# Optimization experiments

Hardware: AMD Instinct MI355X
Metric: run time of the kernel (lower is better)

Reference implementation:

```python
import jax, jax.numpy as jnp
import numpy as np
from jax import lax

BITWIDTH = 7
EPS = 1e-5


def ti_quant(x):
    """TiFloatToInt8: per-tensor int8 quantization with power-of-2 scale."""
    rng = jnp.max(jnp.abs(x))
    bw = jnp.ceil(jnp.log2(rng))
    exp = bw - BITWIDTH
    q = jnp.clip(jnp.round(x * 2.0 ** (BITWIDTH - bw)), -128.0, 127.0)
    return q, exp


def ti_conv(xv, xe, wv, we, pad):
    """TiConv2d: integer conv (simulated in f32, all values int-valued),
    int32 accumulate, then shift back to 8 bits; exponents add."""
    acc = lax.conv_general_dilated(
        xv, wv, window_strides=(1, 1), padding=[(pad, pad), (pad, pad)],
        dimension_numbers=("NCHW", "OIHW", "NCHW"))
    rng = jnp.max(jnp.abs(acc))
    bw = jnp.ceil(jnp.log2(rng))
    shift = jnp.maximum(bw - BITWIDTH, 0.0)
    q = jnp.clip(jnp.round(acc * 2.0 ** (-shift)), -128.0, 127.0)
    return q, xe + we + shift


def batchnorm(x, gamma, beta):
    # training-mode BN: batch statistics over (N, H, W)
    mean = jnp.mean(x, axis=(0, 2, 3), keepdims=True)
    var = jnp.var(x, axis=(0, 2, 3), keepdims=True)
    g = gamma[None, :, None, None]
    b = beta[None, :, None, None]
    return g * (x - mean) * lax.rsqrt(var + EPS) + b


def setup_inputs() -> dict:
    key = jax.random.key(0)
    k0, k1, k2, k3, k4 = jax.random.split(key, 5)
    B, Cin, Cout, H, W = 32, 128, 256, 56, 56
    x_val = jax.random.randint(k0, (B, Cin, H, W), -128, 128, dtype=jnp.int32)
    x_exp = jnp.zeros((), jnp.float32) - 7.0
    wDW = jnp.round(jnp.clip(jax.random.normal(k1, (Cin, Cin, 3, 3), jnp.float32) * 32.0, -128.0, 127.0))
    wDW_exp = jnp.zeros((), jnp.float32) - 9.0
    wPW = jnp.round(jnp.clip(jax.random.normal(k2, (Cout, Cin, 1, 1), jnp.float32) * 32.0, -128.0, 127.0))
    wPW_exp = jnp.zeros((), jnp.float32) - 9.0
    gamma1 = jnp.ones((Cin,), jnp.float32) + 0.1 * jax.random.normal(k3, (Cin,), jnp.float32)
    beta1 = jnp.zeros((Cin,), jnp.float32)
    gamma2 = jnp.ones((Cout,), jnp.float32) + 0.1 * jax.random.normal(k4, (Cout,), jnp.float32)
    beta2 = jnp.zeros((Cout,), jnp.float32)
    return {"x_val": x_val, "x_exp": x_exp, "wDW": wDW, "wDW_exp": wDW_exp,
            "wPW": wPW, "wPW_exp": wPW_exp, "gamma1": gamma1, "beta1": beta1,
            "gamma2": gamma2, "beta2": beta2}


def reference(x_val, x_exp, wDW, wDW_exp, wPW, wPW_exp, gamma1, beta1, gamma2, beta2):
    xv = x_val.astype(jnp.float32)
    # convDW (3x3, in->in, pad=1)
    q, e = ti_conv(xv, x_exp, wDW, wDW_exp, 1)
    # dequant -> bn1 -> quant
    f = batchnorm(q * 2.0 ** e, gamma1, beta1)
    q, e = ti_quant(f)
    # TiReLU on int values
    q = jnp.maximum(q, 0.0)
    # convPW (1x1, in->out)
    q, e = ti_conv(q, e, wPW, wPW_exp, 0)
    # dequant -> bn2 -> quant -> relu
    f = batchnorm(q * 2.0 ** e, gamma2, beta2)
    q, e = ti_quant(f)
    q = jnp.maximum(q, 0.0)
    return q.astype(jnp.int8), e
```

## Files before the change

### kernel.cpp

```cpp
#include <hip/hip_runtime.h>
#include <cstdint>
#include <cstddef>

#define C1 128
#define C2 256
#define Hh 56
#define Wd 56
#define HW 3136
#define NHW 100352
#define N1 ((size_t)12845056)
#define N2 ((size_t)25690112)
#define XPSZ ((size_t)13778944)
#define NREP 8
#define NB1 392

typedef int v4i __attribute__((ext_vector_type(4)));
typedef int v16i __attribute__((ext_vector_type(16)));

static constexpr size_t OFF_XP = 0;
static constexpr size_t OFF_Q1 = XPSZ;
static constexpr size_t OFF_Q3 = OFF_Q1 + N1;
static constexpr size_t OFF_WQ1 = OFF_Q3 + N2;
static constexpr size_t OFF_WQ2 = OFF_WQ1 + 147456;
static constexpr size_t OFF_STATS = OFF_WQ2 + 32768;

struct Stats {
  int absmax1, absmax2, pad0, pad1;
  float scale1, e1, s2, e2;
  float scaleq2, e3, sf, ef;
  int padA[20];
  int tick1, padB[31];
  int tick2, padC[31];
  int tick3, padD[31];
  int sum1[NREP][C1]; unsigned sumsq1[NREP][C1];
  int min1[NREP][C1], max1[NREP][C1];
  float A1[C1], B1c[C1];
  int sum2[NREP][C2]; unsigned sumsq2[NREP][C2];
  int min2[NREP][C2], max2[NREP][C2];
  float A2[C2], B2c[C2];
};

__global__ __launch_bounds__(256) void k_pre(
    const int* __restrict__ x, signed char* __restrict__ xp,
    const float* __restrict__ wDW, signed char* __restrict__ wq1t,
    const float* __restrict__ wPW, signed char* __restrict__ wq2t,
    Stats* st) {
  __shared__ signed char lds[56 * 132];
  int t = threadIdx.x, bid = blockIdx.x;
  if (bid < 1856) {
    int hh = bid % 58, n = bid / 58;
    int* xpw = (int*)(xp + ((size_t)n * 58 + hh) * 7424);
    if (hh == 0 || hh == 57) {
      for (int o = t; o < 1856; o += 256) xpw[o] = 0;
      return;
    }
    int h = hh - 1;
    const int* xb = x + (size_t)n * C1 * HW + h * 56;
    for (int idx = t; idx < 7168; idx += 256) {
      int c = idx / 56, w = idx - c * 56;
      lds[w * 132 + c] = (signed char)xb[(size_t)c * HW + w];
    }
    __syncthreads();
    for (int o = t; o < 1856; o += 256) {
      int kb = o / 232, r = o - kb * 232, ww = r >> 2, cw = r & 3;
      int val = (ww == 0 || ww == 57) ? 0
                : *(const int*)&lds[(ww - 1) * 132 + kb * 16 + cw * 4];
      xpw[o] = val;
    }
    return;
  }
  if (bid < 2432) {
    int idx = (bid - 1856) * 256 + t;
    int co = idx / 1152, r = idx - co * 1152;
    int ci = r / 9, pos = r - ci * 9;
    int k = pos * 128 + ci;
    wq1t[(size_t)(k >> 4) * 2048 + co * 16 + (k & 15)] = (signed char)(int)wDW[idx];
    return;
  }
  if (bid < 2560) {
    int i = (bid - 2432) * 256 + t;
    int co = i >> 7, ci = i & 127;
    wq2t[(size_t)(ci >> 4) * 4096 + co * 16 + (ci & 15)] = (signed char)(int)wPW[i];
    return;
  }
  if (t == 0) {
    st->absmax1 = 0; st->absmax2 = 0;
    st->tick1 = 0; st->tick2 = 0; st->tick3 = 0;
  }
  for (int c = t; c < NREP * C1; c += 256) {
    ((int*)st->sum1)[c] = 0; ((unsigned*)st->sumsq1)[c] = 0u;
    ((int*)st->min1)[c] = 127; ((int*)st->max1)[c] = -128;
  }
  for (int c = t; c < NREP * C2; c += 256) {
    ((int*)st->sum2)[c] = 0; ((unsigned*)st->sumsq2)[c] = 0u;
    ((int*)st->min2)[c] = 127; ((int*)st->max2)[c] = -128;
  }
}

__device__ inline v4i ld16_lds(const signed char* p) {
  const int2* q = (const int2*)p;
  int2 lo = q[0], hi = q[1];
  v4i r; r[0] = lo.x; r[1] = lo.y; r[2] = hi.x; r[3] = hi.y;
  return r;
}

__device__ inline float bn_affine_v(int sum, unsigned sumsq, int mn, int mx,
                                    float g, float b, float e_in,
                                    float* Aout, float* Bout) {
  double meanq = (double)sum / (double)NHW;
  double varq = (double)sumsq / (double)NHW - meanq * meanq;
  float se = exp2f(e_in);
  float mean = (float)meanq * se;
  float var = (float)varq * se * se;
  float rsq = 1.0f / sqrtf(var + 1e-5f);
  float Avv = g * se * rsq;
  float Bvv = b - g * mean * rsq;
  *Aout = Avv; *Bout = Bvv;
  return fmaxf(fabsf(Avv * (float)mn + Bvv), fabsf(Avv * (float)mx + Bvv));
}

__device__ inline void conv1_mfma(const signed char* __restrict__ xp,
                                  const signed char* __restrict__ wq1t,
                                  int bx, int t, v16i a1[2][4]) {
  int lane = t & 63, wave = t >> 6;
  int half = lane >> 5, l31 = lane & 31;
  size_t g0 = (size_t)bx * 256;

  const signed char* ab[2];
#pragma unroll
  for (int i = 0; i < 2; ++i) {
    size_t gm = g0 + wave * 64 + i * 32 + l31;
    int n = (int)(gm / HW);
    int p = (int)(gm - (size_t)n * HW);
    int h = p / 56, w = p - h * 56;
    ab[i] = xp + ((size_t)n * 58 + h) * 7424 + w * 16 + half * 928;
  }
  const signed char* bb[4];
#pragma unroll
  for (int j = 0; j < 4; ++j)
    bb[j] = wq1t + (size_t)(j * 32 + l31) * 16 + half * 2048;

#pragma unroll
  for (int i = 0; i < 2; ++i)
#pragma unroll
    for (int j = 0; j < 4; ++j)
#pragma unroll
      for (int r = 0; r < 16; ++r) a1[i][j][r] = 0;

#pragma unroll
  for (int pos = 0; pos < 9; ++pos) {
    int kh = pos / 3, kw = pos - kh * 3;
    const signed char* a0p = ab[0] + kh * 7424 + kw * 16;
    const signed char* a1p = ab[1] + kh * 7424 + kw * 16;
#pragma unroll
    for (int kb = 0; kb < 8; kb += 2) {
      v4i af0 = *(const v4i*)(a0p + kb * 928);
      v4i af1 = *(const v4i*)(a1p + kb * 928);
      v4i bf[4];
#pragma unroll
      for (int j = 0; j < 4; ++j)
        bf[j] = *(const v4i*)(bb[j] + pos * 16384 + kb * 2048);
#pragma unroll
      for (int j = 0; j < 4; ++j) {
        a1[0][j] = __builtin_amdgcn_mfma_i32_32x32x32_i8(af0, bf[j], a1[0][j], 0, 0, 0);
        a1[1][j] = __builtin_amdgcn_mfma_i32_32x32x32_i8(af1, bf[j], a1[1][j], 0, 0, 0);
      }
    }
  }
}

__global__ __launch_bounds__(256, 2) void k_conv1f(
    const signed char* __restrict__ xp, const signed char* __restrict__ wq1t,
    signed char* __restrict__ q1, Stats* st,
    const float* __restrict__ x_exp, const float* __restrict__ wDW_exp,
    const float* __restrict__ gamma1, const float* __restrict__ beta1) {
  __shared__ int reda[4];
  __shared__ int vbro;
  __shared__ int qti[256 * 34];
  __shared__ int psum[C1], psq[C1], pmn[C1], pmx[C1];
  __shared__ float redc[2];
  __shared__ int lastf;
  signed char* qt = (signed char*)qti;
  int t = threadIdx.x, lane = t & 63, wave = t >> 6;
  int half = lane >> 5, l31 = lane & 31;
  int rep = blockIdx.x & (NREP - 1);

  v16i a1[2][4];
  conv1_mfma(xp, wq1t, blockIdx.x, t, a1);

  int am = 0;
#pragma unroll
  for (int i = 0; i < 2; ++i)
#pragma unroll
    for (int j = 0; j < 4; ++j)
#pragma unroll
      for (int r = 0; r < 16; ++r) am = max(am, abs(a1[i][j][r]));
  for (int off = 32; off; off >>= 1) am = max(am, __shfl_down(am, off, 64));
  if (lane == 0) reda[wave] = am;
  if (t < C1) { psum[t] = 0; psq[t] = 0; pmn[t] = 127; pmx[t] = -128; }
  __syncthreads();
  if (t == 0)
    atomicMax(&st->absmax1, max(max(reda[0], reda[1]), max(reda[2], reda[3])));
  __syncthreads();

  if (t == 0) {
    atomicAdd(&st->tick1, 1);
    while (atomicAdd(&st->tick1, 0) < NB1)
      __builtin_amdgcn_s_sleep(8);
    vbro = atomicAdd(&st->absmax1, 0);
  }
  __syncthreads();

  int v1 = vbro;
  int pw = 31 - __clz(v1 | 1);
  int bw = ((v1 & (v1 - 1)) == 0) ? pw : pw + 1;
  int sh = max(bw - 7, 0);
  float scale1 = exp2f((float)(-sh));
  float e1 = x_exp[0] + wDW_exp[0] + (float)sh;
  if (blockIdx.x == 0 && t == 0) st->e1 = e1;

#pragma unroll
  for (int j = 0; j < 4; ++j) {
    int sj = 0, sqj = 0, mnj = 127, mxj = -128;
    int c = j * 32 + l31;
#pragma unroll
    for (int i = 0; i < 2; ++i)
#pragma unroll
      for (int reg = 0; reg < 16; ++reg) {
        int av = a1[i][j][reg];
        int row = (reg & 3) + 8 * (reg >> 2) + 4 * half;
        int pix = wave * 64 + i * 32 + row;
        float r = rintf((float)av * scale1);
        r = fminf(fmaxf(r, -128.f), 127.f);
        int qi = (int)r;
        qt[pix * 136 + c] = (signed char)qi;
        sj += qi; sqj += qi * qi; mnj = min(mnj, qi); mxj = max(mxj, qi);
      }
    sj += __shfl_down(sj, 32, 64);
    sqj += __shfl_down(sqj, 32, 64);
    mnj = min(mnj, __shfl_down(mnj, 32, 64));
    mxj = max(mxj, __shfl_down(mxj, 32, 64));
    if (half == 0) {
      atomicAdd(&psum[c], sj); atomicAdd(&psq[c], sqj);
      atomicMin(&pmn[c], mnj); atomicMax(&pmx[c], mxj);
    }
  }
  __syncthreads();
  if (t < C1) {
    atomicAdd(&st->sum1[rep][t], psum[t]);
    atomicAdd(&st->sumsq1[rep][t], (unsigned)psq[t]);
    atomicMin(&st->min1[rep][t], pmn[t]);
    atomicMax(&st->max1[rep][t], pmx[t]);
  }
  int* q1w = (int*)(q1 + (size_t)blockIdx.x * 256 * 128);
  for (int idx = t; idx < 8192; idx += 256)
    q1w[idx] = qti[(idx >> 5) * 34 + (idx & 31)];

  __syncthreads();
  if (t == 0) lastf = (atomicAdd(&st->tick3, 1) == NB1 - 1);
  __syncthreads();
  if (lastf) {
    if (t < C1) {
      int sm = 0; unsigned sq = 0; int mn = 127, mx = -128;
#pragma unroll
      for (int r2 = 0; r2 < NREP; ++r2) {
        sm += atomicAdd(&st->sum1[r2][t], 0);
        sq += atomicAdd(&st->sumsq1[r2][t], 0u);
        mn = min(mn, atomicMin(&st->min1[r2][t], 127));
        mx = max(mx, atomicMax(&st->max1[r2][t], -128));
      }
      float cand = bn_affine_v(sm, sq, mn, mx, gamma1[t], beta1[t], e1,
                               &st->A1[t], &st->B1c[t]);
      for (int off = 32; off; off >>= 1) cand = fmaxf(cand, __shfl_down(cand, off, 64));
      if ((t & 63) == 0) redc[t >> 6] = cand;
    }
    __syncthreads();
    if (t == 0) {
      float rng = fmaxf(redc[0], redc[1]);
      float bwv = ceilf(log2f(rng));
      st->s2 = exp2f(7.0f - bwv);
      st->e2 = bwv - 7.0f;
    }
  }
}

template <int STORE>
__global__ __launch_bounds__(256, 2) void k_conv2t(
    const signed char* __restrict__ q1, const signed char* __restrict__ wq2t,
    signed char* __restrict__ q3, Stats* st, const float* __restrict__ wPW_exp,
    const float* __restrict__ gamma2, const float* __restrict__ beta2,
    float* __restrict__ out) {
  __shared__ __align__(16) signed char wq2s[32768];
  __shared__ int qti[128 * 34];
  __shared__ int psum[C2], psq[C2], pmn[C2], pmx[C2];
  __shared__ int reda[4];
  __shared__ float red2[4];
  __shared__ int lastf;
  signed char* qt = (signed char*)qti;

  int t = threadIdx.x, lane = t & 63, wave = t >> 6;
  int half = lane >> 5, l31 = lane & 31;
  size_t g0 = (size_t)blockIdx.x * 128;
  int rep = blockIdx.x & (NREP - 1);

  v4i wtmp[8];
#pragma unroll
  for (int i = 0; i < 8; ++i)
    wtmp[i] = *(const v4i*)(wq2t + i * 4096 + t * 16);
  const int* q1w = (const int*)(q1 + g0 * 128);
  int qv[16];
#pragma unroll
  for (int k = 0; k < 16; ++k) qv[k] = q1w[k * 256 + t];

  if (STORE) { psum[t] = 0; psq[t] = 0; pmn[t] = 127; pmx[t] = -128; }

  int c4 = t & 31;
  float Av[4], Bv[4];
#pragma unroll
  for (int jj = 0; jj < 4; ++jj) {
    Av[jj] = st->A1[c4 * 4 + jj];
    Bv[jj] = st->B1c[c4 * 4 + jj];
  }
  float s2 = st->s2;

#pragma unroll
  for (int i = 0; i < 8; ++i)
    *(v4i*)(wq2s + i * 4096 + t * 16) = wtmp[i];

#pragma unroll
  for (int k = 0; k < 16; ++k) {
    int v = qv[k];
    int pix = (k * 256 + t) >> 5;
    int outv = 0;
#pragma unroll
    for (int jj = 0; jj < 4; ++jj) {
      int b = (signed char)(v >> (8 * jj));
      float y = Av[jj] * (float)b + Bv[jj];
      float r = rintf(y * s2);
      r = fminf(fmaxf(r, -128.f), 127.f);
      r = fmaxf(r, 0.f);
      outv |= ((int)r & 0xff) << (8 * jj);
    }
    qti[pix * 34 + c4] = outv;
  }
  __syncthreads();

  v16i acc[8];
#pragma unroll
  for (int j = 0; j < 8; ++j)
#pragma unroll
    for (int r = 0; r < 16; ++r) acc[j][r] = 0;

#pragma unroll
  for (int ks = 0; ks < 4; ++ks) {
    v4i af = ld16_lds(&qt[(wave * 32 + l31) * 136 + half * 16 + ks * 32]);
#pragma unroll
    for (int j = 0; j < 8; ++j) {
      v4i bf = *(const v4i*)(wq2s + (size_t)(ks * 2 + half) * 4096 + (j * 32 + l31) * 16);
      acc[j] = __builtin_amdgcn_mfma_i32_32x32x32_i8(af, bf, acc[j], 0, 0, 0);
    }
  }

  if (STORE == 0) {
    int am2 = 0;
#pragma unroll
    for (int j = 0; j < 8; ++j)
#pragma unroll
      for (int r = 0; r < 16; ++r) am2 = max(am2, abs(acc[j][r]));
    for (int off = 32; off; off >>= 1) am2 = max(am2, __shfl_down(am2, off, 64));
    if (lane == 0) reda[wave] = am2;
    __syncthreads();
    if (t == 0)
      atomicMax(&st->absmax2, max(max(reda[0], reda[1]), max(reda[2], reda[3])));
  } else {
    int v2 = st->absmax2;
    int pw = 31 - __clz(v2 | 1);
    int bw = ((v2 & (v2 - 1)) == 0) ? pw : pw + 1;
    int sh2 = max(bw - 7, 0);
    float scale2 = exp2f((float)(-sh2));
    float e3 = st->e2 + wPW_exp[0] + (float)sh2;
    if (blockIdx.x == 0 && t == 0) st->e3 = e3;
    int* q3w = (int*)(q3 + (size_t)blockIdx.x * 32768);
#pragma unroll
    for (int j = 0; j < 8; ++j) {
      int c = j * 32 + l31;
      int sj = 0, sqj = 0, mnj = 127, mxj = -128;
#pragma unroll
      for (int rg = 0; rg < 4; ++rg) {
        int pk = 0;
#pragma unroll
        for (int b = 0; b < 4; ++b) {
          float r = rintf((float)acc[j][4 * rg + b] * scale2);
          r = fminf(fmaxf(r, -128.f), 127.f);
          int qi = (int)r;
          pk |= (qi & 0xff) << (8 * b);
          sj += qi; sqj += qi * qi; mnj = min(mnj, qi); mxj = max(mxj, qi);
        }
        q3w[((wave * 8 + j) * 4 + rg) * 64 + lane] = pk;
      }
      sj += __shfl_down(sj, 32, 64);
      sqj += __shfl_down(sqj, 32, 64);
      mnj = min(mnj, __shfl_down(mnj, 32, 64));
      mxj = max(mxj, __shfl_down(mxj, 32, 64));
      if (half == 0) {
        atomicAdd(&psum[c], sj); atomicAdd(&psq[c], sqj);
        atomicMin(&pmn[c], mnj); atomicMax(&pmx[c], mxj);
      }
    }
    __syncthreads();
    atomicAdd(&st->sum2[rep][t], psum[t]);
    atomicAdd(&st->sumsq2[rep][t], (unsigned)psq[t]);
    atomicMin(&st->min2[rep][t], pmn[t]);
    atomicMax(&st->max2[rep][t], pmx[t]);

    __syncthreads();
    if (t == 0) lastf = (atomicAdd(&st->tick2, 1) == 783);
    __syncthreads();
    if (lastf) {
      int sm = 0; unsigned sq = 0; int mn = 127, mx = -128;
#pragma unroll
      for (int r2 = 0; r2 < NREP; ++r2) {
        sm += atomicAdd(&st->sum2[r2][t], 0);
        sq += atomicAdd(&st->sumsq2[r2][t], 0u);
        mn = min(mn, atomicMin(&st->min2[r2][t], 127));
        mx = max(mx, atomicMax(&st->max2[r2][t], -128));
      }
      float cand = bn_affine_v(sm, sq, mn, mx, gamma2[t], beta2[t], e3,
                               &st->A2[t], &st->B2c[t]);
      for (int off = 32; off; off >>= 1) cand = fmaxf(cand, __shfl_down(cand, off, 64));
      if (lane == 0) red2[wave] = cand;
      __syncthreads();
      if (t == 0) {
        float rng = fmaxf(fmaxf(red2[0], red2[1]), fmaxf(red2[2], red2[3]));
        float bwv = ceilf(log2f(rng));
        st->sf = exp2f(7.0f - bwv);
        st->ef = bwv - 7.0f;
        out[N2] = bwv - 7.0f;
      }
    }
  }
}

__global__ __launch_bounds__(256) void k_out(
    const signed char* __restrict__ q3, const Stats* __restrict__ st,
    float* __restrict__ out) {
  __shared__ int ldsc[256 * 17];
  int t = threadIdx.x, lane = t & 63, wave = t >> 6;
  int bid = blockIdx.x;
  size_t g0 = (size_t)bid * 64;
  int n = (int)(g0 / HW), p0 = (int)(g0 - (size_t)n * HW);
  const int* q3r = (const int*)(q3 + (size_t)(bid >> 1) * 32768) + (bid & 1) * 4096;
#pragma unroll
  for (int k = 0; k < 16; ++k) {
    int i = k * 256 + t;
    int ln = i & 63, rg = (i >> 6) & 3, j = (i >> 8) & 7, wv = (i >> 11) & 1;
    int v = q3r[i];
    int c = j * 32 + (ln & 31);
    int psub = wv * 8 + 2 * rg + (ln >> 5);
    ldsc[c * 17 + psub] = v;
  }
  __syncthreads();
  float sf = st->sf;
  float* ob = out + (size_t)n * C2 * HW + p0 + lane;
#pragma unroll
  for (int cg = 0; cg < 64; ++cg) {
    int c = wave * 64 + ((cg + wave * 16) & 63);
    int vv = ldsc[c * 17 + (lane >> 2)];
    float y = st->A2[c] * (float)((signed char)(vv >> (8 * (lane & 3)))) + st->B2c[c];
    float r = rintf(y * sf);
    r = fminf(fmaxf(r, -128.f), 127.f);
    ob[(size_t)c * HW] = fmaxf(r, 0.f);
  }
}

extern "C" void kernel_launch(void* const* d_in, const int* in_sizes, int n_in,
                              void* d_out, int out_size, void* d_ws, size_t ws_size,
                              hipStream_t stream) {
  const int* x = (const int*)d_in[0];
  const float* x_exp = (const float*)d_in[1];
  const float* wDW = (const float*)d_in[2];
  const float* wDW_exp = (const float*)d_in[3];
  const float* wPW = (const float*)d_in[4];
  const float* wPW_exp = (const float*)d_in[5];
  const float* gamma1 = (const float*)d_in[6];
  const float* beta1 = (const float*)d_in[7];
  const float* gamma2 = (const float*)d_in[8];
  const float* beta2 = (const float*)d_in[9];
  float* out = (float*)d_out;

  char* ws = (char*)d_ws;
  signed char* xp2 = (signed char*)(ws + OFF_XP);
  signed char* q1 = (signed char*)(ws + OFF_Q1);
  signed char* q3 = (signed char*)(ws + OFF_Q3);
  signed char* wq1t = (signed char*)(ws + OFF_WQ1);
  signed char* wq2t = (signed char*)(ws + OFF_WQ2);
  Stats* st = (Stats*)(ws + OFF_STATS);

  hipLaunchKernelGGL(k_pre, dim3(2561), dim3(256), 0, stream,
                     x, xp2, wDW, wq1t, wPW, wq2t, st);
  hipLaunchKernelGGL(k_conv1f, dim3(NB1), dim3(256), 0, stream,
                     xp2, wq1t, q1, st, x_exp, wDW_exp, gamma1, beta1);
  hipLaunchKernelGGL(HIP_KERNEL_NAME(k_conv2t<0>), dim3(784), dim3(256), 0, stream,
                     q1, wq2t, q3, st, wPW_exp, gamma2, beta2, out);
  hipLaunchKernelGGL(HIP_KERNEL_NAME(k_conv2t<1>), dim3(784), dim3(256), 0, stream,
                     q1, wq2t, q3, st, wPW_exp, gamma2, beta2, out);
  hipLaunchKernelGGL(k_out, dim3(1568), dim3(256), 0, stream, q3, st, out);
}
```

Before: 262.8 us.

## Fuse two conv2 passes into one persistent kernel with grid-wide spin barrier

Replaces the two launches of the pointwise conv (absmax pass, then store pass) with a single kernel of 392 blocks, each handling 256 pixels. Blocks compute the absmax, meet at a global atomic-counter barrier, then recompute the MFMA GEMM and quantize/store with per-channel stats. This removes one launch and the second re-read and re-transform of q1. It also drops the LDS staging of weights in favor of direct global loads. The spin barrier relies on all 392 blocks being co-resident, and the GEMM is still computed twice.

Result: no change. 265.9 us (+1.2%).

```diff
diff --git a/kernel.cpp b/kernel.cpp
--- a/kernel.cpp
+++ b/kernel.cpp
@@ -13,6 +13,7 @@
 #define XPSZ ((size_t)13778944)
 #define NREP 8
 #define NB1 392
+#define NB2C 392
 
 typedef int v4i __attribute__((ext_vector_type(4)));
 typedef int v16i __attribute__((ext_vector_type(16)));
@@ -32,6 +33,7 @@
   int tick1, padB[31];
   int tick2, padC[31];
   int tick3, padD[31];
+  int tick4, padE[31];
   int sum1[NREP][C1]; unsigned sumsq1[NREP][C1];
   int min1[NREP][C1], max1[NREP][C1];
   float A1[C1], B1c[C1];
@@ -85,7 +87,7 @@
   }
   if (t == 0) {
     st->absmax1 = 0; st->absmax2 = 0;
-    st->tick1 = 0; st->tick2 = 0; st->tick3 = 0;
+    st->tick1 = 0; st->tick2 = 0; st->tick3 = 0; st->tick4 = 0;
   }
   for (int c = t; c < NREP * C1; c += 256) {
     ((int*)st->sum1)[c] = 0; ((unsigned*)st->sumsq1)[c] = 0u;
@@ -284,35 +286,24 @@
   }
 }
 
-template <int STORE>
-__global__ __launch_bounds__(256, 2) void k_conv2t(
+__global__ __launch_bounds__(256, 2) void k_conv2f(
     const signed char* __restrict__ q1, const signed char* __restrict__ wq2t,
     signed char* __restrict__ q3, Stats* st, const float* __restrict__ wPW_exp,
     const float* __restrict__ gamma2, const float* __restrict__ beta2,
     float* __restrict__ out) {
-  __shared__ __align__(16) signed char wq2s[32768];
-  __shared__ int qti[128 * 34];
+  __shared__ int qti[256 * 34];
   __shared__ int psum[C2], psq[C2], pmn[C2], pmx[C2];
   __shared__ int reda[4];
   __shared__ float red2[4];
-  __shared__ int lastf;
+  __shared__ int vbro, lastf;
   signed char* qt = (signed char*)qti;
 
   int t = threadIdx.x, lane = t & 63, wave = t >> 6;
   int half = lane >> 5, l31 = lane & 31;
-  size_t g0 = (size_t)blockIdx.x * 128;
+  size_t g0 = (size_t)blockIdx.x * 256;
   int rep = blockIdx.x & (NREP - 1);
 
-  v4i wtmp[8];
-#pragma unroll
-  for (int i = 0; i < 8; ++i)
-    wtmp[i] = *(const v4i*)(wq2t + i * 4096 + t * 16);
-  const int* q1w = (const int*)(q1 + g0 * 128);
-  int qv[16];
-#pragma unroll
-  for (int k = 0; k < 16; ++k) qv[k] = q1w[k * 256 + t];
-
-  if (STORE) { psum[t] = 0; psq[t] = 0; pmn[t] = 127; pmx[t] = -128; }
+  psum[t] = 0; psq[t] = 0; pmn[t] = 127; pmx[t] = -128;
 
   int c4 = t & 31;
   float Av[4], Bv[4];
@@ -322,15 +313,12 @@
     Bv[jj] = st->B1c[c4 * 4 + jj];
   }
   float s2 = st->s2;
-
-#pragma unroll
-  for (int i = 0; i < 8; ++i)
-    *(v4i*)(wq2s + i * 4096 + t * 16) = wtmp[i];
-
-#pragma unroll
-  for (int k = 0; k < 16; ++k) {
-    int v = qv[k];
-    int pix = (k * 256 + t) >> 5;
+  const int* q1w = (const int*)(q1 + g0 * 128);
+#pragma unroll
+  for (int k = 0; k < 32; ++k) {
+    int idx = k * 256 + t;
+    int v = q1w[idx];
+    int pix = idx >> 5;
     int outv = 0;
 #pragma unroll
     for (int jj = 0; jj < 4; ++jj) {
@@ -345,98 +333,135 @@
   }
   __syncthreads();
 
-  v16i acc[8];
-#pragma unroll
-  for (int j = 0; j < 8; ++j)
-#pragma unroll
-    for (int r = 0; r < 16; ++r) acc[j][r] = 0;
-
-#pragma unroll
-  for (int ks = 0; ks < 4; ++ks) {
-    v4i af = ld16_lds(&qt[(wave * 32 + l31) * 136 + half * 16 + ks * 32]);
-#pragma unroll
-    for (int j = 0; j < 8; ++j) {
-      v4i bf = *(const v4i*)(wq2s + (size_t)(ks * 2 + half) * 4096 + (j * 32 + l31) * 16);
-      acc[j] = __builtin_amdgcn_mfma_i32_32x32x32_i8(af, bf, acc[j], 0, 0, 0);
-    }
-  }
-
-  if (STORE == 0) {
-    int am2 = 0;
-#pragma unroll
-    for (int j = 0; j < 8; ++j)
-#pragma unroll
-      for (int r = 0; r < 16; ++r) am2 = max(am2, abs(acc[j][r]));
-    for (int off = 32; off; off >>= 1) am2 = max(am2, __shfl_down(am2, off, 64));
-    if (lane == 0) reda[wave] = am2;
+  int am2 = 0;
+#pragma unroll
+  for (int pg = 0; pg < 2; ++pg) {
+    int prow = pg * 128 + wave * 32 + l31;
+#pragma unroll
+    for (int h2 = 0; h2 < 2; ++h2) {
+      v16i acc[4];
+#pragma unroll
+      for (int j = 0; j < 4; ++j)
+#pragma unroll
+        for (int r = 0; r < 16; ++r) acc[j][r] = 0;
+#pragma unroll
+      for (int ks = 0; ks < 4; ++ks) {
+        v4i af = ld16_lds(&qt[prow * 136 + half * 16 + ks * 32]);
+#pragma unroll
+        for (int j = 0; j < 4; ++j) {
+          v4i bf = *(const v4i*)(wq2t + (size_t)(ks * 2 + half) * 4096 +
+                                 ((h2 * 4 + j) * 32 + l31) * 16);
+          acc[j] = __builtin_amdgcn_mfma_i32_32x32x32_i8(af, bf, acc[j], 0, 0, 0);
+        }
+      }
+#pragma unroll
+      for (int j = 0; j < 4; ++j)
+#pragma unroll
+        for (int r = 0; r < 16; ++r) am2 = max(am2, abs(acc[j][r]));
+    }
+  }
+  for (int off = 32; off; off >>= 1) am2 = max(am2, __shfl_down(am2, off, 64));
+  if (lane == 0) reda[wave] = am2;
+  __syncthreads();
+  if (t == 0)
+    atomicMax(&st->absmax2, max(max(reda[0], reda[1]), max(reda[2], reda[3])));
+  __syncthreads();
+
+  if (t == 0) {
+    atomicAdd(&st->tick4, 1);
+    while (atomicAdd(&st->tick4, 0) < NB2C)
+      __builtin_amdgcn_s_sleep(8);
+    vbro = atomicAdd(&st->absmax2, 0);
+  }
+  __syncthreads();
+
+  int v2 = vbro;
+  int pw = 31 - __clz(v2 | 1);
+  int bw = ((v2 & (v2 - 1)) == 0) ? pw : pw + 1;
+  int sh2 = max(bw - 7, 0);
+  float scale2 = exp2f((float)(-sh2));
+  float e3 = st->e2 + wPW_exp[0] + (float)sh2;
+  if (blockIdx.x == 0 && t == 0) st->e3 = e3;
+
+#pragma unroll
+  for (int pg = 0; pg < 2; ++pg) {
+    int prow = pg * 128 + wave * 32 + l31;
+    int* q3w = (int*)(q3 + (size_t)blockIdx.x * 65536 + pg * 32768);
+#pragma unroll
+    for (int h2 = 0; h2 < 2; ++h2) {
+      v16i acc[4];
+#pragma unroll
+      for (int j = 0; j < 4; ++j)
+#pragma unroll
+        for (int r = 0; r < 16; ++r) acc[j][r] = 0;
+#pragma unroll
+      for (int ks = 0; ks < 4; ++ks) {
+        v4i af = ld16_lds(&qt[prow * 136 + half * 16 + ks * 32]);
+#pragma unroll
+        for (int j = 0; j < 4; ++j) {
+          v4i bf = *(const v4i*)(wq2t + (size_t)(ks * 2 + half) * 4096 +
+                                 ((h2 * 4 + j) * 32 + l31) * 16);
+          acc[j] = __builtin_amdgcn_mfma_i32_32x32x32_i8(af, bf, acc[j], 0, 0, 0);
+        }
+      }
+#pragma unroll
+      for (int j = 0; j < 4; ++j) {
+        int jg = h2 * 4 + j;
+        int c = jg * 32 + l31;
+        int sj = 0, sqj = 0, mnj = 127, mxj = -128;
+#pragma unroll
+        for (int rg = 0; rg < 4; ++rg) {
+          int pk = 0;
+#pragma unroll
+          for (int b = 0; b < 4; ++b) {
+            float r = rintf((float)acc[j][4 * rg + b] * scale2);
+            r = fminf(fmaxf(r, -128.f), 127.f);
+            int qi = (int)r;
+            pk |= (qi & 0xff) << (8 * b);
+            sj += qi; sqj += qi * qi; mnj = min(mnj, qi); mxj = max(mxj, qi);
+          }
+          q3w[((wave * 8 + jg) * 4 + rg) * 64 + lane] = pk;
+        }
+        sj += __shfl_down(sj, 32, 64);
+        sqj += __shfl_down(sqj, 32, 64);
+        mnj = min(mnj, __shfl_down(mnj, 32, 64));
+        mxj = max(mxj, __shfl_down(mxj, 32, 64));
+        if (half == 0) {
+          atomicAdd(&psum[c], sj); atomicAdd(&psq[c], sqj);
+          atomicMin(&pmn[c], mnj); atomicMax(&pmx[c], mxj);
+        }
+      }
+    }
+  }
+  __syncthreads();
+  atomicAdd(&st->sum2[rep][t], psum[t]);
+  atomicAdd(&st->sumsq2[rep][t], (unsigned)psq[t]);
+  atomicMin(&st->min2[rep][t], pmn[t]);
+  atomicMax(&st->max2[rep][t], pmx[t]);
+
+  __syncthreads();
+  if (t == 0) lastf = (atomicAdd(&st->tick2, 1) == NB2C - 1);
+  __syncthreads();
+  if (lastf) {
+    int sm = 0; unsigned sq = 0; int mn = 127, mx = -128;
+#pragma unroll
+    for (int r2 = 0; r2 < NREP; ++r2) {
+      sm += atomicAdd(&st->sum2[r2][t], 0);
+      sq += atomicAdd(&st->sumsq2[r2][t], 0u);
+      mn = min(mn, atomicMin(&st->min2[r2][t], 127));
+      mx = max(mx, atomicMax(&st->max2[r2][t], -128));
+    }
+    float cand = bn_affine_v(sm, sq, mn, mx, gamma2[t], beta2[t], e3,
+                             &st->A2[t], &st->B2c[t]);
+    for (int off = 32; off; off >>= 1) cand = fmaxf(cand, __shfl_down(cand, off, 64));
+    if (lane == 0) red2[wave] = cand;
     __syncthreads();
-    if (t == 0)
-      atomicMax(&st->absmax2, max(max(reda[0], reda[1]), max(reda[2], reda[3])));
-  } else {
-    int v2 = st->absmax2;
-    int pw = 31 - __clz(v2 | 1);
-    int bw = ((v2 & (v2 - 1)) == 0) ? pw : pw + 1;
-    int sh2 = max(bw - 7, 0);
-    float scale2 = exp2f((float)(-sh2));
-    float e3 = st->e2 + wPW_exp[0] + (float)sh2;
-    if (blockIdx.x == 0 && t == 0) st->e3 = e3;
-    int* q3w = (int*)(q3 + (size_t)blockIdx.x * 32768);
-#pragma unroll
-    for (int j = 0; j < 8; ++j) {
-      int c = j * 32 + l31;
-      int sj = 0, sqj = 0, mnj = 127, mxj = -128;
-#pragma unroll
-      for (int rg = 0; rg < 4; ++rg) {
-        int pk = 0;
-#pragma unroll
-        for (int b = 0; b < 4; ++b) {
-          float r = rintf((float)acc[j][4 * rg + b] * scale2);
-          r = fminf(fmaxf(r, -128.f), 127.f);
-          int qi = (int)r;
-          pk |= (qi & 0xff) << (8 * b);
-          sj += qi; sqj += qi * qi; mnj = min(mnj, qi); mxj = max(mxj, qi);
-        }
-        q3w[((wave * 8 + j) * 4 + rg) * 64 + lane] = pk;
-      }
-      sj += __shfl_down(sj, 32, 64);
-      sqj += __shfl_down(sqj, 32, 64);
-      mnj = min(mnj, __shfl_down(mnj, 32, 64));
-      mxj = max(mxj, __shfl_down(mxj, 32, 64));
-      if (half == 0) {
-        atomicAdd(&psum[c], sj); atomicAdd(&psq[c], sqj);
-        atomicMin(&pmn[c], mnj); atomicMax(&pmx[c], mxj);
-      }
-    }
-    __syncthreads();
-    atomicAdd(&st->sum2[rep][t], psum[t]);
-    atomicAdd(&st->sumsq2[rep][t], (unsigned)psq[t]);
-    atomicMin(&st->min2[rep][t], pmn[t]);
-    atomicMax(&st->max2[rep][t], pmx[t]);
-
-    __syncthreads();
-    if (t == 0) lastf = (atomicAdd(&st->tick2, 1) == 783);
-    __syncthreads();
-    if (lastf) {
-      int sm = 0; unsigned sq = 0; int mn = 127, mx = -128;
-#pragma unroll
-      for (int r2 = 0; r2 < NREP; ++r2) {
-        sm += atomicAdd(&st->sum2[r2][t], 0);
-        sq += atomicAdd(&st->sumsq2[r2][t], 0u);
-        mn = min(mn, atomicMin(&st->min2[r2][t], 127));
-        mx = max(mx, atomicMax(&st->max2[r2][t], -128));
-      }
-      float cand = bn_affine_v(sm, sq, mn, mx, gamma2[t], beta2[t], e3,
-                               &st->A2[t], &st->B2c[t]);
-      for (int off = 32; off; off >>= 1) cand = fmaxf(cand, __shfl_down(cand, off, 64));
-      if (lane == 0) red2[wave] = cand;
-      __syncthreads();
-      if (t == 0) {
-        float rng = fmaxf(fmaxf(red2[0], red2[1]), fmaxf(red2[2], red2[3]));
-        float bwv = ceilf(log2f(rng));
-        st->sf = exp2f(7.0f - bwv);
-        st->ef = bwv - 7.0f;
-        out[N2] = bwv - 7.0f;
-      }
+    if (t == 0) {
+      float rng = fmaxf(fmaxf(red2[0], red2[1]), fmaxf(red2[2], red2[3]));
+      float bwv = ceilf(log2f(rng));
+      st->sf = exp2f(7.0f - bwv);
+      st->ef = bwv - 7.0f;
+      out[N2] = bwv - 7.0f;
     }
   }
 }
@@ -500,9 +525,7 @@
                      x, xp2, wDW, wq1t, wPW, wq2t, st);
   hipLaunchKernelGGL(k_conv1f, dim3(NB1), dim3(256), 0, stream,
                      xp2, wq1t, q1, st, x_exp, wDW_exp, gamma1, beta1);
-  hipLaunchKernelGGL(HIP_KERNEL_NAME(k_conv2t<0>), dim3(784), dim3(256), 0, stream,
-                     q1, wq2t, q3, st, wPW_exp, gamma2, beta2, out);
-  hipLaunchKernelGGL(HIP_KERNEL_NAME(k_conv2t<1>), dim3(784), dim3(256), 0, stream,
+  hipLaunchKernelGGL(k_conv2f, dim3(NB2C), dim3(256), 0, stream,
                      q1, wq2t, q3, st, wPW_exp, gamma2, beta2, out);
   hipLaunchKernelGGL(k_out, dim3(1568), dim3(256), 0, stream, q3, st, out);
 }
```
